# Kernel tuning notes

Hardware: AMD Instinct MI355X
Metric: run time of the kernel (lower is better)

## Reference

```python
import jax, jax.numpy as jnp
import numpy as np

IMG = 640
NUM_CLASSES = 80
MAX_MATCHES = 10  # == num_gt (required by the module's one-hot loop broadcast)
ALPHA = 0.5
BETA = 6.0
EPS = 1e-05
KEPS = 1e-07  # keras backend epsilon


def _make_anchor_points():
    pts = []
    for s in (8, 16, 32):
        n = IMG // s
        xs = (jnp.arange(n, dtype=jnp.float32) + 0.5) * s
        gx, gy = jnp.meshgrid(xs, xs, indexing='xy')
        pts.append(jnp.stack([gx, gy], axis=-1).reshape(-1, 2))
    return jnp.concatenate(pts, axis=0)  # [8400, 2]


def setup_inputs() -> dict:
    key = jax.random.key(0)
    ks = jax.random.split(key, 6)
    B, A, C, G = 32, 8400, NUM_CLASSES, 10
    anchors = _make_anchor_points()                                  # [A,2]
    scores = jax.random.uniform(ks[0], (B, A, C), dtype=jnp.float32)
    # predicted boxes roughly centered on anchors
    ctr = anchors[None] + 8.0 * jax.random.normal(ks[1], (B, A, 2), dtype=jnp.float32)
    wh = 8.0 + 56.0 * jax.random.uniform(ks[2], (B, A, 2), dtype=jnp.float32)
    decode_bboxes = jnp.concatenate([ctr - wh / 2, ctr + wh / 2], axis=-1)  # [B,A,4]
    # ground-truth boxes (xyxy within image)
    gmin = jax.random.uniform(ks[3], (B, G, 2), dtype=jnp.float32) * (IMG - 170.0)
    gwh = 20.0 + 150.0 * jax.random.uniform(ks[4], (B, G, 2), dtype=jnp.float32)
    gt_bboxes = jnp.concatenate([gmin, gmin + gwh], axis=-1)         # [B,G,4]
    gt_labels = jax.random.randint(ks[5], (B, G), 0, C, dtype=jnp.int32)
    gt_mask = jnp.ones((B, G, 1), dtype=bool)
    return {"scores": scores, "decode_bboxes": decode_bboxes, "anchors": anchors,
            "gt_labels": gt_labels, "gt_bboxes": gt_bboxes, "gt_mask": gt_mask}


def compute_ciou(b1, b2):
    # b1 [B,G,1,4], b2 [B,1,A,4] -> [B,G,A]
    x1a, y1a, x2a, y2a = (b1[..., i] for i in range(4))
    x1b, y1b, x2b, y2b = (b2[..., i] for i in range(4))
    w1 = x2a - x1a
    h1 = y2a - y1a + 1e-05
    w2 = x2b - x1b
    h2 = y2b - y1b + 1e-05
    inter = (jnp.maximum(jnp.minimum(x2a, x2b) - jnp.maximum(x1a, x1b), 0.0) *
             jnp.maximum(jnp.minimum(y2a, y2b) - jnp.maximum(y1a, y1b), 0.0))
    union = w1 * h1 + w2 * h2 - inter + 1e-05
    iou = inter / (union + 1e-05)
    cw = jnp.maximum(x2a, x2b) - jnp.minimum(x1a, x1b)
    ch = jnp.maximum(y2a, y2b) - jnp.minimum(y1a, y1b)
    c2 = cw ** 2 + ch ** 2 + KEPS
    rho2 = (((x1a + x2a) - (x1b + x2b)) / 2) ** 2 + (((y1a + y2a) - (y1b + y2b)) / 2) ** 2
    v = (4.0 / np.pi ** 2) * (jnp.arctan(w2 / h2) - jnp.arctan(w1 / h1)) ** 2
    alpha = v / (v - iou + (1.0 + KEPS))
    return iou - (rho2 / c2 + v * alpha)


def reference(scores, decode_bboxes, anchors, gt_labels, gt_bboxes, gt_mask):
    B, A, C = scores.shape
    G = gt_bboxes.shape[1]
    # per-gt class score for every anchor: [B,G,A]
    idx = jnp.broadcast_to(jnp.maximum(gt_labels, 0)[:, None, :], (B, A, G))
    bbox_scores = jnp.take_along_axis(scores, idx, axis=-1)          # [B,A,G]
    bbox_scores = jnp.transpose(bbox_scores, (0, 2, 1))              # [B,G,A]
    overlaps = compute_ciou(gt_bboxes[:, :, None, :], decode_bboxes[:, None, :, :])  # [B,G,A]
    align = jnp.power(bbox_scores, ALPHA) * jnp.power(overlaps, BETA)
    align = jnp.where(gt_mask, align, 0.0)
    # anchor center strictly inside gt box: [B,G,A]
    in_box = jnp.all((gt_bboxes[:, :, None, :2] < anchors) &
                     (gt_bboxes[:, :, None, 2:] > anchors), axis=-1)
    align = jnp.where(in_box, align, 0.0)
    cand_vals, cand_idxs = jax.lax.top_k(align, MAX_MATCHES)         # [B,G,K]
    cand_idxs = jnp.where(cand_vals > 0, cand_idxs, -1)
    # faithful to original loop: sum_k one_hot(cand_idxs[:, k], A)  -> sum over axis 1
    matched = jax.nn.one_hot(cand_idxs, A, dtype=overlaps.dtype).sum(axis=1)  # [B,K,A]==[B,G,A]
    overlaps = overlaps * matched
    gt_match = jnp.argmax(overlaps, axis=1).astype(jnp.int32)        # [B,A]
    match_mask = jnp.max(overlaps, axis=1) > 0                       # [B,A]
    bbox_labels = jnp.take_along_axis(
        gt_bboxes, jnp.broadcast_to(gt_match[:, :, None], (B, A, 4)), axis=1)  # [B,A,4]
    bbox_labels = jnp.where(match_mask[:, :, None], bbox_labels, -1.0)
    class_labels = jnp.take_along_axis(gt_labels, gt_match, axis=1)  # [B,A]
    class_labels = jnp.where(match_mask, class_labels, -1)
    class_labels = jax.nn.one_hot(class_labels, C, dtype=scores.dtype)  # [B,A,C]
    align = align * matched
    max_align = jnp.max(align, axis=-1, keepdims=True)               # [B,G,1]
    max_overlap = jnp.max(overlaps, axis=-1, keepdims=True)          # [B,G,1]
    norm_align = jnp.max(align * max_overlap / (max_align + EPS), axis=-2)  # [B,A]
    class_labels = class_labels * norm_align[:, :, None]
    fg_mask = (gt_match > -1).astype(jnp.float32)                    # [B,A]
    return (jax.lax.stop_gradient(bbox_labels.reshape(-1, A, 4)),
            jax.lax.stop_gradient(class_labels),
            jax.lax.stop_gradient(fg_mask))
```

## Files before the change

kernel.cpp:

```cpp
#include <hip/hip_runtime.h>
#include <math.h>

#define A_TOT 8400
#define NGT 10
#define NCLS 80
#define KTOP 10
#define NB_BATCH 32
#define NWAVE 132
#define ROWKEYS (NWAVE * KTOP)

typedef unsigned int u32;
typedef unsigned long long u64;

struct GtP {
    float x1, y1, x2, y2;
    float area1;
    float at1;
    float sx, sy;
    int lab;
    int rawlab;
};

__device__ __forceinline__ void compute_pair(
    const GtP& g,
    float x1b, float y1b, float x2b, float y2b,
    float area2, float at2, float sxb, float syb,
    float ax, float ay, float score,
    float* ciou_out, float* align_out)
{
    float iw = fmaxf(fminf(g.x2, x2b) - fmaxf(g.x1, x1b), 0.0f);
    float ih = fmaxf(fminf(g.y2, y2b) - fmaxf(g.y1, y1b), 0.0f);
    float inter = iw * ih;
    float uni = g.area1 + area2 - inter + 1e-5f;
    float iou = inter / (uni + 1e-5f);
    float cw = fmaxf(g.x2, x2b) - fminf(g.x1, x1b);
    float ch = fmaxf(g.y2, y2b) - fminf(g.y1, y1b);
    float c2 = cw * cw + ch * ch + 1e-7f;
    float dx = (g.sx - sxb) * 0.5f;
    float dy = (g.sy - syb) * 0.5f;
    float rho2 = dx * dx + dy * dy;
    float dat = at2 - g.at1;
    float v = 0.40528473456935109f * (dat * dat);
    float alpha = v / (v - iou + 1.0000001f);
    float o = iou - (rho2 / c2 + v * alpha);
    *ciou_out = o;
    bool inb = (g.x1 < ax) && (g.y1 < ay) && (g.x2 > ax) && (g.y2 > ay);
    float o2 = o * o;
    float p6 = o2 * o2 * o2;
    *align_out = inb ? (sqrtf(score) * p6) : 0.0f;
}

__device__ __forceinline__ void load_gt(const float* gbox, const int* glab, int b, int g, GtP* out)
{
    const float* p = gbox + ((size_t)b * NGT + g) * 4;
    float x1 = p[0], y1 = p[1], x2 = p[2], y2 = p[3];
    out->x1 = x1; out->y1 = y1; out->x2 = x2; out->y2 = y2;
    float w1 = x2 - x1;
    float h1 = y2 - y1 + 1e-5f;
    out->area1 = w1 * h1;
    out->at1 = atanf(w1 / h1);
    out->sx = x1 + x2;
    out->sy = y1 + y2;
    int lb = glab[b * NGT + g];
    out->rawlab = lb;
    out->lab = lb > 0 ? lb : 0;
}

__device__ __forceinline__ u64 shfl_xor_u64(u64 x, int m)
{
    u32 lo = (u32)x, hi = (u32)(x >> 32);
    lo = __shfl_xor(lo, m, 64);
    hi = __shfl_xor(hi, m, 64);
    return ((u64)hi << 32) | lo;
}

__global__ __launch_bounds__(256) void k_alignfill(
    const float* __restrict__ scores, const float* __restrict__ dec,
    const float* __restrict__ anch, const int* __restrict__ glab,
    const float* __restrict__ gbox,
    u64* __restrict__ keys, float4* __restrict__ outv)
{
    __shared__ GtP sg[NGT];
    int b = blockIdx.y, tid = threadIdx.x;
    if (tid < NGT) load_gt(gbox, glab, b, tid, &sg[tid]);
    __syncthreads();

    {
        const int NBv = 268800;
        const int NCv = 5644800;
        const int NTv = 5712000;
        int lin = (b * 33 + blockIdx.x) * 256 + tid;
        const int stride = 33 * NB_BATCH * 256;
        for (int i = lin; i < NTv; i += stride) {
            float v = (i < NBv) ? -1.0f : (i < NCv ? 0.0f : 1.0f);
            outv[i] = make_float4(v, v, v, v);
        }
    }

    int a = blockIdx.x * 256 + tid;
    bool valid = (a < A_TOT);
    int asafe = valid ? a : 0;
    int lane = tid & 63;
    int wglob = blockIdx.x * 4 + (tid >> 6);

    float4 bx = ((const float4*)dec)[(size_t)b * A_TOT + asafe];
    float x1b = bx.x, y1b = bx.y, x2b = bx.z, y2b = bx.w;
    float w2 = x2b - x1b;
    float h2 = y2b - y1b + 1e-5f;
    float area2 = w2 * h2;
    float at2 = atanf(w2 / h2);
    float sxb = x1b + x2b, syb = y1b + y2b;
    float2 ap = ((const float2*)anch)[asafe];
    const float* srow = scores + ((size_t)b * A_TOT + asafe) * NCLS;

    #pragma unroll
    for (int g = 0; g < NGT; ++g) {
        bool inb = valid &&
                   (sg[g].x1 < ap.x) && (sg[g].y1 < ap.y) &&
                   (sg[g].x2 > ap.x) && (sg[g].y2 > ap.y);
        float al = 0.0f;
        if (inb) {
            float ci;
            compute_pair(sg[g], x1b, y1b, x2b, y2b, area2, at2, sxb, syb,
                         ap.x, ap.y, srow[sg[g].lab], &ci, &al);
        }
        bool pred = (al > 0.0f);
        u64 key = pred ? (((u64)__float_as_uint(al) << 32) | (u32)(~(u32)a)) : 0ull;
        u64 mask = __ballot(pred);
        int cnt = __popcll(mask);
        u64* slot = keys + ((size_t)((b * NGT + g) * NWAVE + wglob)) * KTOP;
        if (cnt <= KTOP) {
            int rank = __popcll(mask & ((1ull << lane) - 1ull));
            if (pred) slot[rank] = key;
            if (lane >= cnt && lane < KTOP) slot[lane] = 0ull;
        } else {
            u64 cur = key;
            #pragma unroll
            for (int k = 0; k < KTOP; ++k) {
                u64 c = cur;
                #pragma unroll
                for (int off = 1; off <= 32; off <<= 1) {
                    u64 o = shfl_xor_u64(c, off);
                    if (o > c) c = o;
                }
                if (cur == c) cur = 0ull;
                if (lane == 0) slot[k] = c;
            }
        }
    }
}

__global__ __launch_bounds__(640) void k_sel(
    const float* __restrict__ scores, const float* __restrict__ dec,
    const float* __restrict__ anch, const int* __restrict__ glab,
    const float* __restrict__ gbox,
    const u64* __restrict__ keys,
    float* __restrict__ out_bbox, float* __restrict__ out_cls)
{
    __shared__ int cid[100];
    __shared__ GtP sg[NGT];
    __shared__ float aLS[NGT][100];
    __shared__ float oLS[NGT][100];
    __shared__ float Cg[NGT];
    int b = blockIdx.x, tid = threadIdx.x;
    int wid = tid >> 6, lane = tid & 63;

    if (tid < NGT) load_gt(gbox, glab, b, tid, &sg[tid]);

    {
        const u64* e = keys + (size_t)(b * NGT + wid) * ROWKEYS;
        u64 L[10];
        #pragma unroll
        for (int j = 0; j < 10; ++j) L[j] = 0ull;
        for (int i = lane; i < ROWKEYS; i += 64) {
            u64 key = e[i];
            if (key > L[9]) {
                L[9] = key;
                #pragma unroll
                for (int j = 9; j > 0; --j) {
                    u64 x = L[j - 1], y = L[j];
                    if (y > x) { L[j - 1] = y; L[j] = x; }
                }
            }
        }
        #pragma unroll
        for (int k = 0; k < KTOP; ++k) {
            u64 c = L[0];
            #pragma unroll
            for (int off = 1; off <= 32; off <<= 1) {
                u64 o = shfl_xor_u64(c, off);
                if (o > c) c = o;
            }
            if (c != 0ull && L[0] == c) {
                #pragma unroll
                for (int j = 0; j < 9; ++j) L[j] = L[j + 1];
                L[9] = 0ull;
            }
            if (lane == 0) {
                int idx = (int)(~(u32)(c & 0xFFFFFFFFu));
                cid[wid * KTOP + k] = (c != 0ull) ? idx : -1;
            }
        }
    }
    __syncthreads();

    for (int t = tid; t < NGT * 100; t += 640) {
        int g = t / 100, e = t - g * 100;
        int a = cid[e];
        float ci = 0.0f, al = 0.0f;
        if (a >= 0) {
            float4 bx = ((const float4*)dec)[(size_t)b * A_TOT + a];
            float x1b = bx.x, y1b = bx.y, x2b = bx.z, y2b = bx.w;
            float w2 = x2b - x1b;
            float h2 = y2b - y1b + 1e-5f;
            float area2 = w2 * h2;
            float at2 = atanf(w2 / h2);
            float2 ap = ((const float2*)anch)[a];
            float s = scores[((size_t)b * A_TOT + a) * NCLS + sg[g].lab];
            compute_pair(sg[g], x1b, y1b, x2b, y2b, area2, at2,
                         x1b + x2b, y1b + y2b, ap.x, ap.y, s, &ci, &al);
        }
        oLS[g][e] = ci;
        aLS[g][e] = al;
    }
    __syncthreads();

    if (tid < NGT) {
        int j = tid;
        float mA = 0.0f, mO = 0.0f;
        for (int gp = 0; gp < NGT; ++gp) {
            int e = gp * NGT + j;
            int a = cid[e];
            if (a < 0) continue;
            int m = 0;
            for (int gq = 0; gq < NGT; ++gq) m += (cid[gq * NGT + j] == a);
            float fm = (float)m;
            mA = fmaxf(mA, aLS[j][e] * fm);
            mO = fmaxf(mO, oLS[j][e] * fm);
        }
        Cg[j] = mO / (mA + 1e-5f);
    }
    __syncthreads();

    if (tid < 100) {
        int e = tid, a = cid[e];
        if (a >= 0) {
            float best = -INFINITY;
            int bg = 0;
            float nrm = 0.0f;
            #pragma unroll
            for (int g = 0; g < NGT; ++g) {
                int m = 0;
                #pragma unroll
                for (int gq = 0; gq < NGT; ++gq) m += (cid[gq * NGT + g] == a);
                float fm = (float)m;
                float vo = oLS[g][e] * fm;
                if (vo > best) { best = vo; bg = g; }
                nrm = fmaxf(nrm, aLS[g][e] * fm * Cg[g]);
            }
            if (best > 0.0f) {
                float4 bb = make_float4(sg[bg].x1, sg[bg].y1, sg[bg].x2, sg[bg].y2);
                ((float4*)out_bbox)[(size_t)b * A_TOT + a] = bb;
                int rl = sg[bg].rawlab;
                if (rl >= 0 && rl < NCLS)
                    out_cls[((size_t)b * A_TOT + a) * NCLS + rl] = nrm;
            }
        }
    }
}

extern "C" void kernel_launch(void* const* d_in, const int* in_sizes, int n_in,
                              void* d_out, int out_size, void* d_ws, size_t ws_size,
                              hipStream_t stream)
{
    (void)in_sizes; (void)n_in; (void)out_size; (void)ws_size;
    const float* scores = (const float*)d_in[0];
    const float* dec    = (const float*)d_in[1];
    const float* anch   = (const float*)d_in[2];
    const int*   glab   = (const int*)d_in[3];
    const float* gbox   = (const float*)d_in[4];

    float* out      = (float*)d_out;
    float* out_bbox = out;
    float* out_cls  = out + (size_t)NB_BATCH * A_TOT * 4;

    u64* keys = (u64*)d_ws;

    k_alignfill<<<dim3(33, NB_BATCH), 256, 0, stream>>>(scores, dec, anch, glab, gbox,
                                                        keys, (float4*)d_out);
    k_sel      <<<NB_BATCH, 640, 0, stream>>>(scores, dec, anch, glab, gbox,
                                              keys, out_bbox, out_cls);
}
```

Before: 188.9 us.

## Store per-wave candidate lists with counts instead of per-wave top-10 reductions

Each wave now compacts all positive-alignment candidates into a 64-slot segment and records a count, replacing the in-wave top-10 shuffle reduction and zero-padding. The selection kernel walks each segment up to its count rather than scanning fixed 10-key slots. The output fill loop moves after the candidate pass so the dependent keys are written early. This removes the shuffle-heavy path when many lanes match, at the cost of more workspace and a serial per-lane loop in the selection kernel whose length depends on segment occupancy.

```diff
diff --git a/kernel.cpp b/kernel.cpp
--- a/kernel.cpp
+++ b/kernel.cpp
@@ -7,7 +7,7 @@
 #define KTOP 10
 #define NB_BATCH 32
 #define NWAVE 132
-#define ROWKEYS (NWAVE * KTOP)
+#define CAP_W 64
 
 typedef unsigned int u32;
 typedef unsigned long long u64;
@@ -78,24 +78,13 @@
     const float* __restrict__ scores, const float* __restrict__ dec,
     const float* __restrict__ anch, const int* __restrict__ glab,
     const float* __restrict__ gbox,
-    u64* __restrict__ keys, float4* __restrict__ outv)
+    u64* __restrict__ entries, u32* __restrict__ counts,
+    float4* __restrict__ outv)
 {
     __shared__ GtP sg[NGT];
     int b = blockIdx.y, tid = threadIdx.x;
     if (tid < NGT) load_gt(gbox, glab, b, tid, &sg[tid]);
     __syncthreads();
-
-    {
-        const int NBv = 268800;
-        const int NCv = 5644800;
-        const int NTv = 5712000;
-        int lin = (b * 33 + blockIdx.x) * 256 + tid;
-        const int stride = 33 * NB_BATCH * 256;
-        for (int i = lin; i < NTv; i += stride) {
-            float v = (i < NBv) ? -1.0f : (i < NCv ? 0.0f : 1.0f);
-            outv[i] = make_float4(v, v, v, v);
-        }
-    }
 
     int a = blockIdx.x * 256 + tid;
     bool valid = (a < A_TOT);
@@ -125,27 +114,25 @@
                          ap.x, ap.y, srow[sg[g].lab], &ci, &al);
         }
         bool pred = (al > 0.0f);
-        u64 key = pred ? (((u64)__float_as_uint(al) << 32) | (u32)(~(u32)a)) : 0ull;
         u64 mask = __ballot(pred);
-        int cnt = __popcll(mask);
-        u64* slot = keys + ((size_t)((b * NGT + g) * NWAVE + wglob)) * KTOP;
-        if (cnt <= KTOP) {
+        int seg_i = (b * NGT + g) * NWAVE + wglob;
+        if (pred) {
             int rank = __popcll(mask & ((1ull << lane) - 1ull));
-            if (pred) slot[rank] = key;
-            if (lane >= cnt && lane < KTOP) slot[lane] = 0ull;
-        } else {
-            u64 cur = key;
-            #pragma unroll
-            for (int k = 0; k < KTOP; ++k) {
-                u64 c = cur;
-                #pragma unroll
-                for (int off = 1; off <= 32; off <<= 1) {
-                    u64 o = shfl_xor_u64(c, off);
-                    if (o > c) c = o;
-                }
-                if (cur == c) cur = 0ull;
-                if (lane == 0) slot[k] = c;
-            }
+            u64 key = ((u64)__float_as_uint(al) << 32) | (u32)(~(u32)a);
+            entries[(size_t)seg_i * CAP_W + rank] = key;
+        }
+        if (lane == 0) counts[seg_i] = (u32)__popcll(mask);
+    }
+
+    {
+        const int NBv = 268800;
+        const int NCv = 5644800;
+        const int NTv = 5712000;
+        int lin = (b * 33 + blockIdx.x) * 256 + tid;
+        const int stride = 33 * NB_BATCH * 256;
+        for (int i = lin; i < NTv; i += stride) {
+            float v = (i < NBv) ? -1.0f : (i < NCv ? 0.0f : 1.0f);
+            outv[i] = make_float4(v, v, v, v);
         }
     }
 }
@@ -154,7 +141,7 @@
     const float* __restrict__ scores, const float* __restrict__ dec,
     const float* __restrict__ anch, const int* __restrict__ glab,
     const float* __restrict__ gbox,
-    const u64* __restrict__ keys,
+    const u64* __restrict__ entries, const u32* __restrict__ counts,
     float* __restrict__ out_bbox, float* __restrict__ out_cls)
 {
     __shared__ int cid[100];
@@ -168,18 +155,24 @@
     if (tid < NGT) load_gt(gbox, glab, b, tid, &sg[tid]);
 
     {
-        const u64* e = keys + (size_t)(b * NGT + wid) * ROWKEYS;
+        int row = b * NGT + wid;
+        const u32* cnt = counts + (size_t)row * NWAVE;
         u64 L[10];
         #pragma unroll
         for (int j = 0; j < 10; ++j) L[j] = 0ull;
-        for (int i = lane; i < ROWKEYS; i += 64) {
-            u64 key = e[i];
-            if (key > L[9]) {
-                L[9] = key;
-                #pragma unroll
-                for (int j = 9; j > 0; --j) {
-                    u64 x = L[j - 1], y = L[j];
-                    if (y > x) { L[j - 1] = y; L[j] = x; }
+
+        for (int s = lane; s < NWAVE; s += 64) {
+            int n = (int)cnt[s];
+            const u64* seg = entries + ((size_t)row * NWAVE + s) * CAP_W;
+            for (int i = 0; i < n; ++i) {
+                u64 key = seg[i];
+                if (key > L[9]) {
+                    L[9] = key;
+                    #pragma unroll
+                    for (int j = 9; j > 0; --j) {
+                        u64 x = L[j - 1], y = L[j];
+                        if (y > x) { L[j - 1] = y; L[j] = x; }
+                    }
                 }
             }
         }
@@ -284,10 +277,11 @@
     float* out_bbox = out;
     float* out_cls  = out + (size_t)NB_BATCH * A_TOT * 4;
 
-    u64* keys = (u64*)d_ws;
+    u32* counts  = (u32*)d_ws;
+    u64* entries = (u64*)((char*)d_ws + 262144);
 
     k_alignfill<<<dim3(33, NB_BATCH), 256, 0, stream>>>(scores, dec, anch, glab, gbox,
-                                                        keys, (float4*)d_out);
+                                                        entries, counts, (float4*)d_out);
     k_sel      <<<NB_BATCH, 640, 0, stream>>>(scores, dec, anch, glab, gbox,
-                                              keys, out_bbox, out_cls);
-}
+                                              entries, counts, out_bbox, out_cls);
+}
```

Result: slower. 202.1 us (+7.0%).
